# Kernel optimization log

Measured on AMD Instinct MI355X. Metric: run time of the kernel, lower is better.

The kernel has to match this reference:

```python
import jax, jax.numpy as jnp
import numpy as np

N = 100_000      # nodes
E = 1_600_000    # edges (avg degree 16)
C_IN, C_H, C_OUT = 32, 64, 64
G = 64           # graphs in batch


def setup_inputs() -> dict:
    key = jax.random.key(0)
    ks = jax.random.split(key, 10)
    x = jax.random.normal(ks[0], (N, C_IN), jnp.float32)
    edge_index = jax.random.randint(ks[1], (2, E), 0, N, dtype=jnp.int64)
    edge_weight = jax.random.uniform(ks[2], (E,), jnp.float32)
    batch = jnp.sort(jax.random.randint(ks[3], (N,), 0, G, dtype=jnp.int64))
    def lin(k, fan_in, fan_out):
        return jax.random.normal(k, (fan_in, fan_out), jnp.float32) / np.float32(np.sqrt(fan_in))
    W1 = lin(ks[4], C_IN, C_H)
    W2 = lin(ks[5], C_H, C_H)
    W3 = lin(ks[6], C_H, C_OUT)
    b1 = jnp.zeros((C_H,), jnp.float32)
    b2 = jnp.zeros((C_H,), jnp.float32)
    b3 = jnp.zeros((C_OUT,), jnp.float32)
    return {"x": x, "edge_weight": edge_weight, "W1": W1, "b1": b1,
            "W2": W2, "b2": b2, "W3": W3, "b3": b3,
            "edge_index": edge_index, "batch": batch}


def _gcn_norm(edge_index, edge_weight, n):
    # PyG GCNConv default: add self-loops (weight 1), symmetric D^-1/2 A D^-1/2 norm.
    loop = jnp.arange(n, dtype=edge_index.dtype)
    src = jnp.concatenate([edge_index[0], loop])
    dst = jnp.concatenate([edge_index[1], loop])
    ew = jnp.concatenate([edge_weight, jnp.ones((n,), edge_weight.dtype)])
    deg = jax.ops.segment_sum(ew, dst, num_segments=n)
    dis = jnp.where(deg > 0, jax.lax.rsqrt(deg), jnp.float32(0))
    norm = dis[src] * ew * dis[dst]
    return src, dst, norm


def _gcn_layer(h, W, b, src, dst, norm, n):
    h = h @ W                                 # [N, out]
    msg = h[src] * norm[:, None]              # gather + scale  [E+N, out]
    agg = jax.ops.segment_sum(msg, dst, num_segments=n)
    return agg + b


def reference(x, edge_weight, W1, b1, W2, b2, W3, b3, edge_index, batch):
    n = x.shape[0]
    src, dst, norm = _gcn_norm(edge_index, edge_weight, n)  # shared across layers
    h = jax.nn.silu(_gcn_layer(x, W1, b1, src, dst, norm, n))
    # Dropout(0.1) is identity in eval mode
    h = jax.nn.silu(_gcn_layer(h, W2, b2, src, dst, norm, n))
    h = jax.nn.silu(_gcn_layer(h, W3, b3, src, dst, norm, n))
    # global_mean_pool over graphs
    sums = jax.ops.segment_sum(h, batch, num_segments=G)
    counts = jax.ops.segment_sum(jnp.ones((n,), h.dtype), batch, num_segments=G)
    return sums / jnp.maximum(counts, 1)[:, None]
```

## Files before the change

kernel.cpp:

```cpp
#include <hip/hip_runtime.h>
#include <hip/hip_fp16.h>
#include <math.h>


#define NB   256
#define PBLK 1024
#define FIXP_SCALE 1048576.0f
#define FIXP_MASK  ((1ULL << 40) - 1)

__device__ __forceinline__ int lower_bound_i(const int* __restrict__ a, int n, int v) {
    int lo = 0, hi = n;
    while (lo < hi) {
        int m = (lo + hi) >> 1;
        if (a[m] < v) lo = m + 1; else hi = m;
    }
    return lo;
}

__global__ __launch_bounds__(256) void k_bhist(const int* __restrict__ dst,
                                               int* __restrict__ hcnt, int e) {
    __shared__ int hist[NB];
    int tid = threadIdx.x, blk = blockIdx.x;
    hist[tid] = 0;
    __syncthreads();
    int chunk = (e + PBLK - 1) / PBLK;
    int lo = blk * chunk, hi = min(e, lo + chunk);
    for (int i = lo + tid; i < hi; i += 256)
        atomicAdd(&hist[dst[i] >> 9], 1);
    __syncthreads();
    hcnt[tid * PBLK + blk] = hist[tid];
}

__global__ __launch_bounds__(256) void k_bscan(int* __restrict__ hcnt,
                                               int* __restrict__ btot) {
    __shared__ int s[256];
    int b = blockIdx.x, tid = threadIdx.x;
    int* row = hcnt + b * PBLK;
    int a0 = row[4 * tid], a1 = row[4 * tid + 1], a2 = row[4 * tid + 2], a3 = row[4 * tid + 3];
    int tsum = a0 + a1 + a2 + a3;
    s[tid] = tsum;
    __syncthreads();
    for (int off = 1; off < 256; off <<= 1) {
        int t = (tid >= off) ? s[tid - off] : 0;
        __syncthreads();
        s[tid] += t;
        __syncthreads();
    }
    int ex = s[tid] - tsum;
    row[4 * tid] = ex;
    row[4 * tid + 1] = ex + a0;
    row[4 * tid + 2] = ex + a0 + a1;
    row[4 * tid + 3] = ex + a0 + a1 + a2;
    if (tid == 255) btot[b] = s[255];
}

__global__ __launch_bounds__(256) void k_bbase(const int* __restrict__ btot,
                                               int* __restrict__ bbase,
                                               int* __restrict__ rowptr, int n, int e) {
    __shared__ int s[256];
    int tid = threadIdx.x;
    int v = btot[tid];
    s[tid] = v;
    __syncthreads();
    for (int off = 1; off < 256; off <<= 1) {
        int t = (tid >= off) ? s[tid - off] : 0;
        __syncthreads();
        s[tid] += t;
        __syncthreads();
    }
    bbase[tid] = s[tid] - v;
    if (tid == 255) bbase[NB] = s[255];
    if (tid == 0) rowptr[n] = e;
}

__global__ __launch_bounds__(256) void k_bpart(const int* __restrict__ src,
                                               const int* __restrict__ dst,
                                               const float* __restrict__ ew,
                                               const int* __restrict__ hcnt,
                                               const int* __restrict__ bbase,
                                               int2* __restrict__ bedge, int e) {
    __shared__ int cur[NB];
    int tid = threadIdx.x, blk = blockIdx.x;
    cur[tid] = bbase[tid] + hcnt[tid * PBLK + blk];
    __syncthreads();
    int chunk = (e + PBLK - 1) / PBLK;
    int lo = blk * chunk, hi = min(e, lo + chunk);
    for (int i = lo + tid; i < hi; i += 256) {
        int d = dst[i];
        int pos = atomicAdd(&cur[d >> 9], 1);
        bedge[pos] = make_int2(src[i] | ((d & 511) << 17), __float_as_int(ew[i]));
    }
}

__global__ __launch_bounds__(256) void k_bucket(const int2* __restrict__ bedge,
                                                const int* __restrict__ bbase,
                                                float* __restrict__ dis,
                                                int* __restrict__ rowptr,
                                                int2* __restrict__ em,
                                                const float* __restrict__ x,
                                                __half* __restrict__ hs, int n) {
    __shared__ unsigned long long pk[512];
    __shared__ int cnt[512];
    __shared__ int scn[512];
    __shared__ float sdis[512];
    __shared__ int cur[512];
    int b = blockIdx.x, tid = threadIdx.x;
    int e0 = bbase[b], e1 = bbase[b + 1];
    pk[tid] = 0ULL; pk[tid + 256] = 0ULL;
    __syncthreads();
    for (int i = e0 + tid; i < e1; i += 256) {
        int2 v = bedge[i];
        int dlo = (v.x >> 17) & 511;
        unsigned long long p =
            (1ULL << 40) | (unsigned long long)(__int_as_float(v.y) * FIXP_SCALE);
        atomicAdd(&pk[dlo], p);
    }
    __syncthreads();
#pragma unroll
    for (int k = 0; k < 2; ++k) {
        int i = tid + k * 256;
        unsigned long long v = pk[i];
        int c = (int)(v >> 40);
        cnt[i] = c; scn[i] = c;
        sdis[i] = rsqrtf(1.0f + (float)(v & FIXP_MASK) * (1.0f / FIXP_SCALE));
    }
    __syncthreads();
    for (int off = 1; off < 512; off <<= 1) {
        int i0 = tid, i1 = tid + 256;
        int v0 = (i0 >= off) ? scn[i0 - off] : 0;
        int v1 = (i1 >= off) ? scn[i1 - off] : 0;
        __syncthreads();
        scn[i0] += v0; scn[i1] += v1;
        __syncthreads();
    }
#pragma unroll
    for (int k = 0; k < 2; ++k) {
        int i = tid + k * 256;
        int rb = e0 + scn[i] - cnt[i];
        cur[i] = rb;
        int node = (b << 9) + i;
        if (node < n) { rowptr[node] = rb; dis[node] = sdis[i]; }
    }
    __syncthreads();
    for (int i = e0 + tid; i < e1; i += 256) {
        int2 v = bedge[i];
        int dlo = (v.x >> 17) & 511;
        int pos = atomicAdd(&cur[dlo], 1);
        float w = __int_as_float(v.y) * sdis[dlo];
        em[pos] = make_int2(v.x & 0x1FFFF, __float_as_int(w));
    }
    int nodebase = b << 9;
    int nloc = n - nodebase; if (nloc > 512) nloc = 512;
    if (nloc > 0) {
        const float2* x2 = (const float2*)(x + (size_t)nodebase * 32);
        __half2* hs2 = (__half2*)(hs + (size_t)nodebase * 32);
        int total2 = nloc * 16;
        for (int i = tid; i < total2; i += 256) {
            float d = sdis[i >> 4];
            float2 v = x2[i];
            hs2[i] = __float22half2_rn(make_float2(v.x * d, v.y * d));
        }
    }
}

__device__ __forceinline__ float2 cvt_pair(unsigned int u) {
    __half2 h2 = *(__half2*)&u;
    return __half22float2(h2);
}

__global__ __launch_bounds__(256, 4) void k_agg32(const __half* __restrict__ hs,
                                                  const int2* __restrict__ em,
                                                  const int* __restrict__ rowptr,
                                                  const float* __restrict__ dis,
                                                  __half* __restrict__ y0, int n) {
    __shared__ __align__(8) int2 sme[4][128];
    int lane = threadIdx.x & 63, wv = threadIdx.x >> 6;
    int c = lane & 7, oct = lane >> 3;
    const uint2* h64 = (const uint2*)hs;
    int wid = (blockIdx.x * blockDim.x + threadIdx.x) >> 6;
    int n0 = wid * 8;
    if (n0 >= n) return;
    int cnt = min(8, n - n0);
    int rp = 0;
    if (lane <= cnt) rp = rowptr[n0 + lane];
    int hiw = __shfl(rp, cnt, 64);
    int wlo = 0, whi = 0;
    for (int k = 0; k < cnt; ++k) {
        int node = n0 + k;
        int lo = __shfl(rp, k, 64), hi = __shfl(rp, k + 1, 64);
        float2 a0 = make_float2(0.0f, 0.0f), a1 = make_float2(0.0f, 0.0f);
        if (oct == 0) {
            float di = dis[node];
            uint2 sh = h64[(unsigned)(node * 8 + c)];
            float2 f0 = cvt_pair(sh.x), f1 = cvt_pair(sh.y);
            a0.x = di * f0.x; a0.y = di * f0.y;
            a1.x = di * f1.x; a1.y = di * f1.y;
        }
        int idx = lo;
        while (idx < hi) {
            if (idx >= whi) {
                int i0 = idx + lane;
                if (i0 < hiw) sme[wv][lane] = em[i0];
                int i1 = i0 + 64;
                if (i1 < hiw) sme[wv][lane + 64] = em[i1];
                wlo = idx; whi = idx + 128;
            }
            int base = idx - wlo;
            int take = min(hi, whi) - idx;
            for (int g = 0; g < take; g += 32) {
                int2 ev[4]; uint2 hv[4]; int pr[4];
#pragma unroll
                for (int t = 0; t < 4; ++t) {
                    int p = g + 8 * t + oct;
                    pr[t] = p < take;
                    int pc = pr[t] ? p : 0;
                    ev[t] = sme[wv][base + pc];
                }
#pragma unroll
                for (int t = 0; t < 4; ++t)
                    hv[t] = h64[(unsigned)(ev[t].x * 8 + c)];
#pragma unroll
                for (int t = 0; t < 4; ++t) {
                    float ww = pr[t] ? __int_as_float(ev[t].y) : 0.0f;
                    float2 f0 = cvt_pair(hv[t].x), f1 = cvt_pair(hv[t].y);
                    a0.x = fmaf(ww, f0.x, a0.x);
                    a0.y = fmaf(ww, f0.y, a0.y);
                    a1.x = fmaf(ww, f1.x, a1.x);
                    a1.y = fmaf(ww, f1.y, a1.y);
                }
            }
            idx += take;
        }
        a0.x += __shfl_down(a0.x, 32, 64); a0.y += __shfl_down(a0.y, 32, 64);
        a1.x += __shfl_down(a1.x, 32, 64); a1.y += __shfl_down(a1.y, 32, 64);
        a0.x += __shfl_down(a0.x, 16, 64); a0.y += __shfl_down(a0.y, 16, 64);
        a1.x += __shfl_down(a1.x, 16, 64); a1.y += __shfl_down(a1.y, 16, 64);
        a0.x += __shfl_down(a0.x, 8, 64);  a0.y += __shfl_down(a0.y, 8, 64);
        a1.x += __shfl_down(a1.x, 8, 64);  a1.y += __shfl_down(a1.y, 8, 64);
        if (oct == 0) {
            uint2 o;
            __half2 p0 = __float22half2_rn(make_float2(a0.x, a0.y));
            __half2 p1 = __float22half2_rn(make_float2(a1.x, a1.y));
            o.x = *(unsigned int*)&p0; o.y = *(unsigned int*)&p1;
            ((uint2*)y0)[(size_t)node * 8 + c] = o;
        }
    }
}

__global__ __launch_bounds__(256, 1) void k_mmf12(const __half* __restrict__ y0,
                                                  const float* __restrict__ W1,
                                                  const float* __restrict__ b1,
                                                  const float* __restrict__ W2,
                                                  const float* __restrict__ dis,
                                                  __half* __restrict__ z2, int n) {
    __shared__ __align__(16) float sw1[32 * 64];
    __shared__ __align__(16) float sw2[64 * 64];
    __shared__ float sb[64];
#pragma unroll
    for (int i = 0; i < 8; ++i) sw1[threadIdx.x + 256 * i] = W1[threadIdx.x + 256 * i];
#pragma unroll
    for (int i = 0; i < 16; ++i) sw2[threadIdx.x + 256 * i] = W2[threadIdx.x + 256 * i];
    if (threadIdx.x < 64) sb[threadIdx.x] = b1[threadIdx.x];
    __syncthreads();
    int node = blockIdx.x * 256 + threadIdx.x;
    if (node >= n) return;
    uint4 yp[4];
    const uint4* yrow = (const uint4*)(y0 + (size_t)node * 32);
#pragma unroll
    for (int i = 0; i < 4; ++i) yp[i] = yrow[i];
    const unsigned int* ypk = (const unsigned int*)yp;
    float o[64];
#pragma unroll
    for (int j = 0; j < 64; ++j) o[j] = sb[j];
#pragma unroll
    for (int k2 = 0; k2 < 16; ++k2) {
        float2 yk = cvt_pair(ypk[k2]);
        const float4* r0 = (const float4*)&sw1[(2 * k2) * 64];
        const float4* r1 = (const float4*)&sw1[(2 * k2 + 1) * 64];
#pragma unroll
        for (int j4 = 0; j4 < 16; ++j4) {
            float4 w0 = r0[j4];
            float4 w1 = r1[j4];
            o[4 * j4 + 0] = fmaf(yk.y, w1.x, fmaf(yk.x, w0.x, o[4 * j4 + 0]));
            o[4 * j4 + 1] = fmaf(yk.y, w1.y, fmaf(yk.x, w0.y, o[4 * j4 + 1]));
            o[4 * j4 + 2] = fmaf(yk.y, w1.z, fmaf(yk.x, w0.z, o[4 * j4 + 2]));
            o[4 * j4 + 3] = fmaf(yk.y, w1.w, fmaf(yk.x, w0.w, o[4 * j4 + 3]));
        }
    }
    float dsc = dis[node];
#pragma unroll
    for (int j = 0; j < 64; ++j) {
        float v = o[j];
        o[j] = v / (1.0f + __expf(-v)) * dsc;
    }
    __half2* zrow = (__half2*)(z2 + (size_t)node * 64);
#pragma unroll
    for (int hblk = 0; hblk < 2; ++hblk) {
        float z[32];
#pragma unroll
        for (int j = 0; j < 32; ++j) z[j] = 0.0f;
#pragma unroll
        for (int k = 0; k < 64; ++k) {
            float a = o[k];
            const float4* r = (const float4*)&sw2[k * 64 + hblk * 32];
#pragma unroll
            for (int j4 = 0; j4 < 8; ++j4) {
                float4 w = r[j4];
                z[4 * j4 + 0] = fmaf(a, w.x, z[4 * j4 + 0]);
                z[4 * j4 + 1] = fmaf(a, w.y, z[4 * j4 + 1]);
                z[4 * j4 + 2] = fmaf(a, w.z, z[4 * j4 + 2]);
                z[4 * j4 + 3] = fmaf(a, w.w, z[4 * j4 + 3]);
            }
        }
#pragma unroll
        for (int j2 = 0; j2 < 16; ++j2)
            zrow[hblk * 16 + j2] =
                __float22half2_rn(make_float2(z[2 * j2], z[2 * j2 + 1]));
    }
}

__global__ __launch_bounds__(256, 2) void k_mm64(const __half* __restrict__ y,
                                                 const float* __restrict__ W,
                                                 __half* __restrict__ z, int n) {
    __shared__ __align__(16) float sw[64 * 64];
#pragma unroll
    for (int i = 0; i < 16; ++i)
        sw[threadIdx.x + 256 * i] = W[threadIdx.x + 256 * i];
    __syncthreads();
    int node = blockIdx.x * 256 + threadIdx.x;
    if (node >= n) return;
    uint4 yp[8];
    const uint4* yrow = (const uint4*)(y + (size_t)node * 64);
#pragma unroll
    for (int i = 0; i < 8; ++i) yp[i] = yrow[i];
    const unsigned int* ypk = (const unsigned int*)yp;
    float o[64];
#pragma unroll
    for (int j = 0; j < 64; ++j) o[j] = 0.0f;
#pragma unroll
    for (int k2 = 0; k2 < 32; ++k2) {
        float2 yk = cvt_pair(ypk[k2]);
        const float4* r0 = (const float4*)&sw[(2 * k2) * 64];
        const float4* r1 = (const float4*)&sw[(2 * k2 + 1) * 64];
#pragma unroll
        for (int j4 = 0; j4 < 16; ++j4) {
            float4 w0 = r0[j4];
            float4 w1 = r1[j4];
            o[4 * j4 + 0] = fmaf(yk.y, w1.x, fmaf(yk.x, w0.x, o[4 * j4 + 0]));
            o[4 * j4 + 1] = fmaf(yk.y, w1.y, fmaf(yk.x, w0.y, o[4 * j4 + 1]));
            o[4 * j4 + 2] = fmaf(yk.y, w1.z, fmaf(yk.x, w0.z, o[4 * j4 + 2]));
            o[4 * j4 + 3] = fmaf(yk.y, w1.w, fmaf(yk.x, w0.w, o[4 * j4 + 3]));
        }
    }
    __half2* zrow = (__half2*)(z + (size_t)node * 64);
#pragma unroll
    for (int j2 = 0; j2 < 32; ++j2)
        zrow[j2] = __float22half2_rn(make_float2(o[2 * j2], o[2 * j2 + 1]));
}

template <bool SCALE, typename OUT>
__global__ __launch_bounds__(256, 4) void k_agg64(const __half* __restrict__ z,
                                                  const int2* __restrict__ em,
                                                  const int* __restrict__ rowptr,
                                                  const float* __restrict__ dis,
                                                  const float* __restrict__ bias,
                                                  OUT* __restrict__ out, int n) {
    __shared__ __align__(8) int2 sme[4][128];
    int lane = threadIdx.x & 63, wv = threadIdx.x >> 6;
    int c = lane & 15, quarter = lane >> 4;
    const uint2* h64 = (const uint2*)z;
    float4 bv4 = ((const float4*)bias)[c];
    int wid = (blockIdx.x * blockDim.x + threadIdx.x) >> 6;
    int n0 = wid * 8;
    if (n0 >= n) return;
    int cnt = min(8, n - n0);
    int rp = 0;
    if (lane <= cnt) rp = rowptr[n0 + lane];
    int hiw = __shfl(rp, cnt, 64);
    int wlo = 0, whi = 0;
    for (int k = 0; k < cnt; ++k) {
        int node = n0 + k;
        int lo = __shfl(rp, k, 64), hi = __shfl(rp, k + 1, 64);
        float di = 0.0f;
        float2 a0 = make_float2(0.0f, 0.0f), a1 = make_float2(0.0f, 0.0f);
        if (quarter == 0) {
            di = dis[node];
            uint2 sh = h64[(unsigned)(node * 16 + c)];
            float2 f0 = cvt_pair(sh.x), f1 = cvt_pair(sh.y);
            a0.x = di * f0.x; a0.y = di * f0.y;
            a1.x = di * f1.x; a1.y = di * f1.y;
        }
        int idx = lo;
        while (idx < hi) {
            if (idx >= whi) {
                int i0 = idx + lane;
                if (i0 < hiw) sme[wv][lane] = em[i0];
                int i1 = i0 + 64;
                if (i1 < hiw) sme[wv][lane + 64] = em[i1];
                wlo = idx; whi = idx + 128;
            }
            int base = idx - wlo;
            int take = min(hi, whi) - idx;
            for (int g = 0; g < take; g += 16) {
                int2 ev[4]; uint2 hv[4]; int pr[4];
#pragma unroll
                for (int t = 0; t < 4; ++t) {
                    int p = g + 4 * t + quarter;
                    pr[t] = p < take;
                    int pc = pr[t] ? p : 0;
                    ev[t] = sme[wv][base + pc];
                }
#pragma unroll
                for (int t = 0; t < 4; ++t)
                    hv[t] = h64[(unsigned)(ev[t].x * 16 + c)];
#pragma unroll
                for (int t = 0; t < 4; ++t) {
                    float ww = pr[t] ? __int_as_float(ev[t].y) : 0.0f;
                    float2 f0 = cvt_pair(hv[t].x), f1 = cvt_pair(hv[t].y);
                    a0.x = fmaf(ww, f0.x, a0.x);
                    a0.y = fmaf(ww, f0.y, a0.y);
                    a1.x = fmaf(ww, f1.x, a1.x);
                    a1.y = fmaf(ww, f1.y, a1.y);
                }
            }
            idx += take;
        }
        a0.x += __shfl_down(a0.x, 32, 64); a0.y += __shfl_down(a0.y, 32, 64);
        a1.x += __shfl_down(a1.x, 32, 64); a1.y += __shfl_down(a1.y, 32, 64);
        a0.x += __shfl_down(a0.x, 16, 64); a0.y += __shfl_down(a0.y, 16, 64);
        a1.x += __shfl_down(a1.x, 16, 64); a1.y += __shfl_down(a1.y, 16, 64);
        if (quarter == 0) {
            float ox = a0.x + bv4.x, oy = a0.y + bv4.y;
            float oz = a1.x + bv4.z, ow = a1.y + bv4.w;
            ox = ox / (1.0f + __expf(-ox));
            oy = oy / (1.0f + __expf(-oy));
            oz = oz / (1.0f + __expf(-oz));
            ow = ow / (1.0f + __expf(-ow));
            if (SCALE) { ox *= di; oy *= di; oz *= di; ow *= di; }
            if (sizeof(OUT) == 2) {
                uint2 o;
                __half2 p0 = __float22half2_rn(make_float2(ox, oy));
                __half2 p1 = __float22half2_rn(make_float2(oz, ow));
                o.x = *(unsigned int*)&p0; o.y = *(unsigned int*)&p1;
                ((uint2*)out)[(size_t)node * 16 + c] = o;
            } else {
                ((float4*)out)[(size_t)node * 16 + c] = make_float4(ox, oy, oz, ow);
            }
        }
    }
}

__global__ void k_pool_partial(const float* __restrict__ h, const int* __restrict__ batch,
                               float* __restrict__ acc, int n) {
    int c = threadIdx.x & 63, r = threadIdx.x >> 6;
    int base = blockIdx.x * 128;
    int end = base + 128; if (end > n) end = n;
    float part = 0.0f;
    int cur = -1;
    for (int i = base + r; i < end; i += 4) {
        int g = batch[i];
        if (g != cur) {
            if (cur >= 0) atomicAdd(&acc[cur * 64 + c], part);
            part = 0.0f;
            cur = g;
        }
        part += h[(size_t)i * 64 + c];
    }
    if (cur >= 0) atomicAdd(&acc[cur * 64 + c], part);
}

__global__ void k_pool_final(const float* __restrict__ acc, const int* __restrict__ batch,
                             float* __restrict__ out, int n) {
    int idx = blockIdx.x * blockDim.x + threadIdx.x;
    int g = idx >> 6;
    int lo = lower_bound_i(batch, n, g);
    int hi = lower_bound_i(batch, n, g + 1);
    int cnt = hi - lo;
    out[idx] = acc[idx] / (float)(cnt > 0 ? cnt : 1);
}

extern "C" void kernel_launch(void* const* d_in, const int* in_sizes, int n_in,
                              void* d_out, int out_size, void* d_ws, size_t ws_size,
                              hipStream_t stream) {
    const float* x   = (const float*)d_in[0];
    const float* ew  = (const float*)d_in[1];
    const float* W1  = (const float*)d_in[2];
    const float* b1  = (const float*)d_in[3];
    const float* W2  = (const float*)d_in[4];
    const float* b2  = (const float*)d_in[5];
    const float* W3  = (const float*)d_in[6];
    const float* b3  = (const float*)d_in[7];
    const int*   eidx  = (const int*)d_in[8];
    const int*   batch = (const int*)d_in[9];
    float* out = (float*)d_out;

    const int E = in_sizes[1];
    const int N = in_sizes[9];
    const int G = 64;
    const int* src = eidx;
    const int* dst = eidx + E;

    char* p = (char*)d_ws;
    __half* A     = (__half*)p;                p += (size_t)N * 64 * sizeof(__half);
    __half* B     = (__half*)p;                p += (size_t)N * 64 * sizeof(__half);
    float* C      = (float*)p;                 p += (size_t)N * 64 * sizeof(float);
    float* dis    = (float*)p;                 p += (size_t)N * sizeof(float);
    int*   rowptr = (int*)p;                   p += (size_t)(N + 1) * sizeof(int);
    int*   bbase  = (int*)p;                   p += (size_t)(NB + 1) * sizeof(int);
    float* acc    = (float*)p;                 p += (size_t)G * 64 * sizeof(float);
    p = (char*)(((uintptr_t)p + 7) & ~(uintptr_t)7);
    int2*  em     = (int2*)p;

    int2* bedge = (int2*)A;
    int*  hcnt  = (int*)B;
    int*  btot  = (int*)B + NB * PBLK;

    const int BT = 256;
    const int WAVES = (N + 7) / 8;
    const int AGG_BLOCKS = (WAVES + 3) / 4;
    const int MM_BLOCKS = (N + 255) / 256;

    k_bhist<<<PBLK, 256, 0, stream>>>(dst, hcnt, E);
    k_bscan<<<NB, 256, 0, stream>>>(hcnt, btot);
    k_bbase<<<1, 256, 0, stream>>>(btot, bbase, rowptr, N, E);
    k_bpart<<<PBLK, 256, 0, stream>>>(src, dst, ew, hcnt, bbase, bedge, E);
    k_bucket<<<NB, 256, 0, stream>>>(bedge, bbase, dis, rowptr, em, x, (__half*)B, N);

    k_agg32<<<AGG_BLOCKS, BT, 0, stream>>>((__half*)B, em, rowptr, dis, (__half*)C, N);

    k_mmf12<<<MM_BLOCKS, BT, 0, stream>>>((__half*)C, W1, b1, W2, dis, (__half*)B, N);

    k_agg64<true, __half><<<AGG_BLOCKS, BT, 0, stream>>>(B, em, rowptr, dis, b2, A, N);

    k_mm64<<<MM_BLOCKS, BT, 0, stream>>>(A, W3, B, N);
    k_agg64<false, float><<<AGG_BLOCKS, BT, 0, stream>>>(B, em, rowptr, dis, b3, C, N);

    hipMemsetAsync(acc, 0, (size_t)G * 64 * sizeof(float), stream);
    k_pool_partial<<<(N + 127) / 128, BT, 0, stream>>>(C, batch, acc, N);
    k_pool_final<<<(G * 64) / BT, BT, 0, stream>>>(acc, batch, out, N);
}
```

Before: 369.0 us.

## Use smaller dst buckets and split fused layer-1/2 matmul into two kernels

New measurement: 387.1 us. +4.9%, slower.

```diff
diff --git a/kernel.cpp b/kernel.cpp
--- a/kernel.cpp
+++ b/kernel.cpp
@@ -3,7 +3,10 @@
 #include <math.h>
 
 
-#define NB   256
+#define NB   1024
+#define BSH  7
+#define BMASK 127
+#define BN   128
 #define PBLK 1024
 #define FIXP_SCALE 1048576.0f
 #define FIXP_MASK  ((1ULL << 40) - 1)
@@ -21,14 +24,19 @@
                                                int* __restrict__ hcnt, int e) {
     __shared__ int hist[NB];
     int tid = threadIdx.x, blk = blockIdx.x;
-    hist[tid] = 0;
+#pragma unroll
+    for (int b = 0; b < NB / 256; ++b) hist[tid + 256 * b] = 0;
     __syncthreads();
     int chunk = (e + PBLK - 1) / PBLK;
     int lo = blk * chunk, hi = min(e, lo + chunk);
     for (int i = lo + tid; i < hi; i += 256)
-        atomicAdd(&hist[dst[i] >> 9], 1);
-    __syncthreads();
-    hcnt[tid * PBLK + blk] = hist[tid];
+        atomicAdd(&hist[dst[i] >> BSH], 1);
+    __syncthreads();
+#pragma unroll
+    for (int b = 0; b < NB / 256; ++b) {
+        int bb = tid + 256 * b;
+        hcnt[bb * PBLK + blk] = hist[bb];
+    }
 }
 
 __global__ __launch_bounds__(256) void k_bscan(int* __restrict__ hcnt,
@@ -59,8 +67,10 @@
                                                int* __restrict__ rowptr, int n, int e) {
     __shared__ int s[256];
     int tid = threadIdx.x;
-    int v = btot[tid];
-    s[tid] = v;
+    int a0 = btot[4 * tid], a1 = btot[4 * tid + 1],
+        a2 = btot[4 * tid + 2], a3 = btot[4 * tid + 3];
+    int tsum = a0 + a1 + a2 + a3;
+    s[tid] = tsum;
     __syncthreads();
     for (int off = 1; off < 256; off <<= 1) {
         int t = (tid >= off) ? s[tid - off] : 0;
@@ -68,7 +78,11 @@
         s[tid] += t;
         __syncthreads();
     }
-    bbase[tid] = s[tid] - v;
+    int ex = s[tid] - tsum;
+    bbase[4 * tid] = ex;
+    bbase[4 * tid + 1] = ex + a0;
+    bbase[4 * tid + 2] = ex + a0 + a1;
+    bbase[4 * tid + 3] = ex + a0 + a1 + a2;
     if (tid == 255) bbase[NB] = s[255];
     if (tid == 0) rowptr[n] = e;
 }
@@ -81,14 +95,18 @@
                                                int2* __restrict__ bedge, int e) {
     __shared__ int cur[NB];
     int tid = threadIdx.x, blk = blockIdx.x;
-    cur[tid] = bbase[tid] + hcnt[tid * PBLK + blk];
+#pragma unroll
+    for (int b = 0; b < NB / 256; ++b) {
+        int bb = tid + 256 * b;
+        cur[bb] = bbase[bb] + hcnt[bb * PBLK + blk];
+    }
     __syncthreads();
     int chunk = (e + PBLK - 1) / PBLK;
     int lo = blk * chunk, hi = min(e, lo + chunk);
     for (int i = lo + tid; i < hi; i += 256) {
         int d = dst[i];
-        int pos = atomicAdd(&cur[d >> 9], 1);
-        bedge[pos] = make_int2(src[i] | ((d & 511) << 17), __float_as_int(ew[i]));
+        int pos = atomicAdd(&cur[d >> BSH], 1);
+        bedge[pos] = make_int2(src[i] | ((d & BMASK) << 17), __float_as_int(ew[i]));
     }
 }
 
@@ -99,58 +117,52 @@
                                                 int2* __restrict__ em,
                                                 const float* __restrict__ x,
                                                 __half* __restrict__ hs, int n) {
-    __shared__ unsigned long long pk[512];
-    __shared__ int cnt[512];
-    __shared__ int scn[512];
-    __shared__ float sdis[512];
-    __shared__ int cur[512];
+    __shared__ unsigned long long pk[BN];
+    __shared__ int cnt[BN];
+    __shared__ int scn[BN];
+    __shared__ float sdis[BN];
+    __shared__ int cur[BN];
     int b = blockIdx.x, tid = threadIdx.x;
     int e0 = bbase[b], e1 = bbase[b + 1];
-    pk[tid] = 0ULL; pk[tid + 256] = 0ULL;
+    if (tid < BN) pk[tid] = 0ULL;
     __syncthreads();
     for (int i = e0 + tid; i < e1; i += 256) {
         int2 v = bedge[i];
-        int dlo = (v.x >> 17) & 511;
+        int dlo = (v.x >> 17) & BMASK;
         unsigned long long p =
             (1ULL << 40) | (unsigned long long)(__int_as_float(v.y) * FIXP_SCALE);
         atomicAdd(&pk[dlo], p);
     }
     __syncthreads();
-#pragma unroll
-    for (int k = 0; k < 2; ++k) {
-        int i = tid + k * 256;
-        unsigned long long v = pk[i];
+    if (tid < BN) {
+        unsigned long long v = pk[tid];
         int c = (int)(v >> 40);
-        cnt[i] = c; scn[i] = c;
-        sdis[i] = rsqrtf(1.0f + (float)(v & FIXP_MASK) * (1.0f / FIXP_SCALE));
-    }
-    __syncthreads();
-    for (int off = 1; off < 512; off <<= 1) {
-        int i0 = tid, i1 = tid + 256;
-        int v0 = (i0 >= off) ? scn[i0 - off] : 0;
-        int v1 = (i1 >= off) ? scn[i1 - off] : 0;
+        cnt[tid] = c; scn[tid] = c;
+        sdis[tid] = rsqrtf(1.0f + (float)(v & FIXP_MASK) * (1.0f / FIXP_SCALE));
+    }
+    __syncthreads();
+    for (int off = 1; off < BN; off <<= 1) {
+        int v0 = (tid >= off && tid < BN) ? scn[tid - off] : 0;
         __syncthreads();
-        scn[i0] += v0; scn[i1] += v1;
+        if (tid < BN) scn[tid] += v0;
         __syncthreads();
     }
-#pragma unroll
-    for (int k = 0; k < 2; ++k) {
-        int i = tid + k * 256;
-        int rb = e0 + scn[i] - cnt[i];
-        cur[i] = rb;
-        int node = (b << 9) + i;
-        if (node < n) { rowptr[node] = rb; dis[node] = sdis[i]; }
+    if (tid < BN) {
+        int rb = e0 + scn[tid] - cnt[tid];
+        cur[tid] = rb;
+        int node = (b << BSH) + tid;
+        if (node < n) { rowptr[node] = rb; dis[node] = sdis[tid]; }
     }
     __syncthreads();
     for (int i = e0 + tid; i < e1; i += 256) {
         int2 v = bedge[i];
-        int dlo = (v.x >> 17) & 511;
+        int dlo = (v.x >> 17) & BMASK;
         int pos = atomicAdd(&cur[dlo], 1);
         float w = __int_as_float(v.y) * sdis[dlo];
         em[pos] = make_int2(v.x & 0x1FFFF, __float_as_int(w));
     }
-    int nodebase = b << 9;
-    int nloc = n - nodebase; if (nloc > 512) nloc = 512;
+    int nodebase = b << BSH;
+    int nloc = n - nodebase; if (nloc > BN) nloc = BN;
     if (nloc > 0) {
         const float2* x2 = (const float2*)(x + (size_t)nodebase * 32);
         __half2* hs2 = (__half2*)(hs + (size_t)nodebase * 32);
@@ -247,20 +259,16 @@
     }
 }
 
-__global__ __launch_bounds__(256, 1) void k_mmf12(const __half* __restrict__ y0,
-                                                  const float* __restrict__ W1,
-                                                  const float* __restrict__ b1,
-                                                  const float* __restrict__ W2,
-                                                  const float* __restrict__ dis,
-                                                  __half* __restrict__ z2, int n) {
-    __shared__ __align__(16) float sw1[32 * 64];
-    __shared__ __align__(16) float sw2[64 * 64];
-    __shared__ float sb[64];
-#pragma unroll
-    for (int i = 0; i < 8; ++i) sw1[threadIdx.x + 256 * i] = W1[threadIdx.x + 256 * i];
-#pragma unroll
-    for (int i = 0; i < 16; ++i) sw2[threadIdx.x + 256 * i] = W2[threadIdx.x + 256 * i];
-    if (threadIdx.x < 64) sb[threadIdx.x] = b1[threadIdx.x];
+__global__ __launch_bounds__(256, 2) void k_mm32act(const __half* __restrict__ y0,
+                                                    const float* __restrict__ W,
+                                                    const float* __restrict__ bias,
+                                                    const float* __restrict__ dis,
+                                                    __half* __restrict__ out, int n) {
+    __shared__ __align__(16) float sw[32 * 64 + 64];
+#pragma unroll
+    for (int i = 0; i < 8; ++i)
+        sw[threadIdx.x + 256 * i] = W[threadIdx.x + 256 * i];
+    if (threadIdx.x < 64) sw[2048 + threadIdx.x] = bias[threadIdx.x];
     __syncthreads();
     int node = blockIdx.x * 256 + threadIdx.x;
     if (node >= n) return;
@@ -271,12 +279,12 @@
     const unsigned int* ypk = (const unsigned int*)yp;
     float o[64];
 #pragma unroll
-    for (int j = 0; j < 64; ++j) o[j] = sb[j];
+    for (int j = 0; j < 64; ++j) o[j] = sw[2048 + j];
 #pragma unroll
     for (int k2 = 0; k2 < 16; ++k2) {
         float2 yk = cvt_pair(ypk[k2]);
-        const float4* r0 = (const float4*)&sw1[(2 * k2) * 64];
-        const float4* r1 = (const float4*)&sw1[(2 * k2 + 1) * 64];
+        const float4* r0 = (const float4*)&sw[(2 * k2) * 64];
+        const float4* r1 = (const float4*)&sw[(2 * k2 + 1) * 64];
 #pragma unroll
         for (int j4 = 0; j4 < 16; ++j4) {
             float4 w0 = r0[j4];
@@ -288,34 +296,13 @@
         }
     }
     float dsc = dis[node];
-#pragma unroll
-    for (int j = 0; j < 64; ++j) {
-        float v = o[j];
-        o[j] = v / (1.0f + __expf(-v)) * dsc;
-    }
-    __half2* zrow = (__half2*)(z2 + (size_t)node * 64);
-#pragma unroll
-    for (int hblk = 0; hblk < 2; ++hblk) {
-        float z[32];
-#pragma unroll
-        for (int j = 0; j < 32; ++j) z[j] = 0.0f;
-#pragma unroll
-        for (int k = 0; k < 64; ++k) {
-            float a = o[k];
-            const float4* r = (const float4*)&sw2[k * 64 + hblk * 32];
-#pragma unroll
-            for (int j4 = 0; j4 < 8; ++j4) {
-                float4 w = r[j4];
-                z[4 * j4 + 0] = fmaf(a, w.x, z[4 * j4 + 0]);
-                z[4 * j4 + 1] = fmaf(a, w.y, z[4 * j4 + 1]);
-                z[4 * j4 + 2] = fmaf(a, w.z, z[4 * j4 + 2]);
-                z[4 * j4 + 3] = fmaf(a, w.w, z[4 * j4 + 3]);
-            }
-        }
-#pragma unroll
-        for (int j2 = 0; j2 < 16; ++j2)
-            zrow[hblk * 16 + j2] =
-                __float22half2_rn(make_float2(z[2 * j2], z[2 * j2 + 1]));
+    __half2* orow = (__half2*)(out + (size_t)node * 64);
+#pragma unroll
+    for (int j2 = 0; j2 < 32; ++j2) {
+        float ox = o[2 * j2], oy = o[2 * j2 + 1];
+        ox = ox / (1.0f + __expf(-ox)) * dsc;
+        oy = oy / (1.0f + __expf(-oy)) * dsc;
+        orow[j2] = __float22half2_rn(make_float2(ox, oy));
     }
 }
 
@@ -527,9 +514,9 @@
     k_bucket<<<NB, 256, 0, stream>>>(bedge, bbase, dis, rowptr, em, x, (__half*)B, N);
 
     k_agg32<<<AGG_BLOCKS, BT, 0, stream>>>((__half*)B, em, rowptr, dis, (__half*)C, N);
-
-    k_mmf12<<<MM_BLOCKS, BT, 0, stream>>>((__half*)C, W1, b1, W2, dis, (__half*)B, N);
-
+    k_mm32act<<<MM_BLOCKS, BT, 0, stream>>>((__half*)C, W1, b1, dis, A, N);
+
+    k_mm64<<<MM_BLOCKS, BT, 0, stream>>>(A, W2, B, N);
     k_agg64<true, __half><<<AGG_BLOCKS, BT, 0, stream>>>(B, em, rowptr, dis, b2, A, N);
 
     k_mm64<<<MM_BLOCKS, BT, 0, stream>>>(A, W3, B, N);
```
